# Kernel tuning notes

Measured on AMD Instinct MI355X. Metric: run time of the kernel, lower is better.

Reference implementation:

```python
import jax, jax.numpy as jnp
import numpy as np

N = 2048
T = 4000
MAX_SPIKES = 512
V_RESET = 1.0
ALPHA = 0.01


def setup_inputs() -> dict:
    key = jax.random.key(0)
    k1, k2, k3, k4, k5 = jax.random.split(key, 5)
    ts = jnp.arange(T, dtype=jnp.float32) * (1.0 / T)  # [T] grid over [0, 1)
    v0 = 0.1 * jax.random.normal(k1, (N,), dtype=jnp.float32)
    i0 = 0.1 * jax.random.normal(k2, (N,), dtype=jnp.float32)
    ic = jax.random.uniform(k3, (N,), dtype=jnp.float32, minval=0.5, maxval=1.5)
    # _build_w: uniform weights in [0.5, 1), network mask all-False -> no zeroing
    w = jax.random.uniform(k4, (N, N), dtype=jnp.float32, minval=0.5, maxval=1.0)
    mu = jax.random.uniform(k5, (2,), dtype=jnp.float32, minval=0.5, maxval=1.0)
    return {"ts": ts, "v0": v0, "i0": i0, "ic": ic, "w": w, "mu": mu,
            "seed": 0, "max_spikes": MAX_SPIKES}


def reference(ts, v0, i0, ic, w, mu, seed, max_spikes):
    n = v0.shape[0]
    key = jax.random.key(seed)
    k_init, k_trans = jax.random.split(key)
    # s0 = log(U) - alpha  (negative; spike when s crosses 0)
    s0 = jnp.log(jax.random.uniform(k_init, (n,))) - ALPHA
    y0 = jnp.stack([v0, i0, s0], axis=-1)  # [n, 3]

    dts = ts[1:] - ts[:-1]
    steps = jnp.arange(ts.shape[0] - 1)
    tev0 = jnp.full((max_spikes,), jnp.inf, dtype=ts.dtype)
    yev0 = jnp.full((max_spikes, n, 3), jnp.inf, dtype=y0.dtype)
    et0 = jnp.zeros((max_spikes, n), dtype=bool)

    def drift(y):
        v, i, s = y[:, 0], y[:, 1], y[:, 2]
        dv = mu[0] * (i + ic - v)
        di = -mu[1] * i
        ds = jax.nn.softplus(v)  # intensity_fn
        return jnp.stack([dv, di, ds], axis=-1)

    def step(carry, inp):
        y, nsp, tev, yev, et = carry
        t_next, dt, idx = inp
        y1 = y + dt * drift(y)                 # Euler step
        ev = y1[:, 2] >= 0.0                   # cond_fn: y[n, 2] root crossing
        has = jnp.any(ev)
        eidx = jnp.argmax(ev)
        u = jax.random.uniform(jax.random.fold_in(k_trans, idx), (n,))
        # trans_fn: reset v, add weight row to all i, resample s for spikers
        v_t = y1[:, 0] - jnp.where(ev, V_RESET, 0.0)
        i_t = y1[:, 1] + w[eidx]
        s_t = jnp.where(ev, jnp.log(u) - ALPHA, y1[:, 2])
        y2 = jnp.where(has, jnp.stack([v_t, i_t, s_t], axis=-1), y1)
        rec = has & (nsp < max_spikes)
        widx = jnp.minimum(nsp, max_spikes - 1)
        tev = tev.at[widx].set(jnp.where(rec, t_next, tev[widx]))
        yev = yev.at[widx].set(jnp.where(rec, y1, yev[widx]))
        et = et.at[widx].set(jnp.where(rec, ev, et[widx]))
        nsp = nsp + has.astype(jnp.int32)
        return (y2, nsp, tev, yev, et), y2

    init = (y0, jnp.int32(0), tev0, yev0, et0)
    (_, num_spikes, tevents, yevents, event_types), ys_rest = jax.lax.scan(
        step, init, (ts[1:], dts, steps))
    ys = jnp.concatenate([y0[None], ys_rest], axis=0)  # [T, n, 3]
    return ys, tevents, yevents, event_types, num_spikes
```

## Files before the change

### kernel.cpp

```cpp
#include <hip/hip_runtime.h>
#include <stdint.h>

#define XLA_LOG_TAIL_A 1
#define XLA_USE_FMA    0

#if XLA_USE_FMA
#define MADD(a,b,c) __builtin_fmaf((a),(b),(c))
#else
#define MADD(a,b,c) ((a)*(b)+(c))
#endif

#define N_NEUR 2048
#define HALF_N 1024
#define CKPT   125

#define LDS_BARRIER()                                            \
  do {                                                           \
    __asm__ __volatile__("s_waitcnt lgkmcnt(0)" ::: "memory");   \
    __builtin_amdgcn_s_barrier();                                \
    __asm__ __volatile__("" ::: "memory");                       \
  } while (0)

__device__ __forceinline__ uint32_t rotl32(uint32_t x, int r) {
  return (x << r) | (x >> (32 - r));
}

__device__ __forceinline__ void tf2x32(uint32_t k0, uint32_t k1,
                                       uint32_t& x0, uint32_t& x1) {
  const uint32_t k2 = k0 ^ k1 ^ 0x1BD11BDAu;
  x0 += k0; x1 += k1;
#define TF_R(r) { x0 += x1; x1 = rotl32(x1, r); x1 ^= x0; }
  TF_R(13) TF_R(15) TF_R(26) TF_R(6)
  x0 += k1; x1 += k2 + 1u;
  TF_R(17) TF_R(29) TF_R(16) TF_R(24)
  x0 += k2; x1 += k0 + 2u;
  TF_R(13) TF_R(15) TF_R(26) TF_R(6)
  x0 += k0; x1 += k1 + 3u;
  TF_R(17) TF_R(29) TF_R(16) TF_R(24)
  x0 += k1; x1 += k2 + 4u;
  TF_R(13) TF_R(15) TF_R(26) TF_R(6)
  x0 += k2; x1 += k0 + 5u;
#undef TF_R
}

__device__ __forceinline__ float u01_from_bits(uint32_t bits) {
#pragma clang fp contract(off)
  float f = __uint_as_float((bits >> 9) | 0x3f800000u);
  return f - 1.0f;
}

__device__ __forceinline__ float xla_log(float xin) {
#pragma clang fp contract(off)
  float t0 = fmaxf(xin, __uint_as_float(0x00800000u));
  uint32_t bits = __float_as_uint(t0);
  int em = (int)(bits >> 23) - 127;
  t0 = __uint_as_float((bits & 0x807fffffu) | 0x3f000000u);
  float e = 1.0f + (float)em;
  const bool mlt = t0 < (float)0.707106781186547524;
  float tmp1 = mlt ? t0 : 0.0f;
  t0 = t0 - 1.0f;
  e = e - (mlt ? 1.0f : 0.0f);
  t0 = t0 + tmp1;
  float x2 = t0 * t0;
  float x3 = x2 * t0;
  float y  = MADD(t0, (float)7.0376836292E-2, (float)-1.1514610310E-1);
  float ya = MADD(t0, (float)-1.2420140846E-1, (float)1.4249322787E-1);
  float yb = MADD(t0, (float)2.0000714765E-1, (float)-2.4999993993E-1);
  y  = MADD(y,  t0, (float)1.1676998740E-1);
  ya = MADD(ya, t0, (float)-1.6668057665E-1);
  yb = MADD(yb, t0, (float)3.3333331174E-1);
  y  = MADD(y, x3, ya);
  y  = MADD(y, x3, yb);
  y  = y * x3;
  float ey1 = e * (float)-2.12194440e-4;
  float hx2 = x2 * 0.5f;
  y = y + ey1;
  t0 = t0 - hx2;
  float ey2 = e * (float)0.693359375;
#if XLA_LOG_TAIL_A
  t0 = t0 + y;
  t0 = t0 + ey2;
#else
  t0 = t0 + ey2;
  t0 = t0 + y;
#endif
  if (xin == 0.0f) return -__builtin_inff();
  return t0;
}

__device__ __forceinline__ float xla_exp(float xin) {
#pragma clang fp contract(off)
  float x = fmaxf(xin, (float)-88.3762626647949);
  x = fminf(x, (float)88.3762626647950);
  float fx = floorf(MADD(x, (float)1.44269504088896341, 0.5f));
  float tmp = (float)0.693359375 * fx;
  float z = (float)-2.12194440e-4 * fx;
  x = x - tmp;
  x = x - z;
  z = x * x;
  float y = MADD(x, (float)1.9875691500E-4, (float)1.3981999507E-3);
  y = MADD(y, x, (float)8.3334519073E-3);
  y = MADD(y, x, (float)4.1665795894E-2);
  y = MADD(y, x, (float)1.6666665459E-1);
  y = MADD(y, x, (float)5.0000001201E-1);
  y = MADD(y, z, x);
  y = 1.0f + y;
  int n = (int)fx;
  float p2n = __uint_as_float((uint32_t)(n + 127) << 23);
  return fmaxf(y * p2n, xin);
}

__device__ __forceinline__ float xla_log1p(float x) {
#pragma clang fp contract(off)
  float fl = xla_log(x + 1.0f);
  float fs = ((-0.5f * x) + 1.0f) * x;
  return (fabsf(x) < (float)1e-4) ? fs : fl;
}

__device__ __forceinline__ float softplus_xla(float v) {
#pragma clang fp contract(off)
  if (v >= 16.0f) return v;
  float a = fabsf(v);
  float ex = xla_exp(-a);
  float lp = xla_log1p(ex);
  return fmaxf(v, 0.0f) + lp;
}

__global__ void snn_init(float* __restrict__ out, size_t inf_base,
                         size_t inf_cnt, size_t zero_cnt) {
  size_t i = (size_t)blockIdx.x * blockDim.x + threadIdx.x;
  size_t stride = (size_t)gridDim.x * blockDim.x;
  size_t total = inf_cnt + zero_cnt;
  for (size_t k = i; k < total; k += stride) {
    out[inf_base + k] = (k < inf_cnt) ? __builtin_inff() : 0.0f;
  }
}

__global__ __launch_bounds__(1024)
void snn_pre(const int* __restrict__ seedp, float* __restrict__ sres) {
#pragma clang fp contract(off)
  const int step = blockIdx.x;
  const int t = threadIdx.x;
  uint32_t seed = (uint32_t)seedp[0];
  uint32_t a0 = 0u, a1 = 2u; tf2x32(0u, seed, a0, a1);
  uint32_t b0 = 1u, b1 = 3u; tf2x32(0u, seed, b0, b1);
  uint32_t f0 = 0u, f1 = (uint32_t)step; tf2x32(a1, b1, f0, f1);
  uint32_t d0 = (uint32_t)t, d1 = (uint32_t)(t + HALF_N);
  tf2x32(f0, f1, d0, d1);
  float srA = xla_log(u01_from_bits(d0)) - 0.01f;
  float srB = xla_log(u01_from_bits(d1)) - 0.01f;
  sres[(size_t)step * N_NEUR + t] = srA;
  sres[(size_t)step * N_NEUR + HALF_N + t] = srB;
}

__global__ __launch_bounds__(1024, 1)
void snn_evt(const float* __restrict__ ts, const float* __restrict__ v0,
             const float* __restrict__ i0, const float* __restrict__ ic,
             const float* __restrict__ w, const float* __restrict__ mu,
             const int* __restrict__ seedp, const float* __restrict__ sres,
             uint32_t* __restrict__ spk, float* __restrict__ out, int T, int MS) {
#pragma clang fp contract(off)
  const int tid = threadIdx.x;
  const int nb = tid * 2;
  const int lane = tid & 63;

  float* ys   = out;
  float* tev  = out + (size_t)T * N_NEUR * 3;
  float* yev  = tev + (size_t)MS;
  float* etv  = yev + (size_t)MS * N_NEUR * 3;
  float* nspp = etv + (size_t)MS * N_NEUR;

  uint32_t seed = (uint32_t)seedp[0];
  uint32_t a0 = 0u, a1 = 2u; tf2x32(0u, seed, a0, a1);
  uint32_t b0 = 1u, b1 = 3u; tf2x32(0u, seed, b0, b1);
  const uint32_t ki0 = a0, ki1 = b0;

  float vv0, vv1, ipd0, ipd1, ss0, ss1, icv0, icv1;
  { float2 x = *(const float2*)&v0[nb]; vv0 = x.x; vv1 = x.y; }
  { float2 x = *(const float2*)&i0[nb]; ipd0 = x.x; ipd1 = x.y; }
  { float2 x = *(const float2*)&ic[nb]; icv0 = x.x; icv1 = x.y; }
  {
    uint32_t c0 = (uint32_t)(nb < HALF_N ? nb : nb - HALF_N);
    uint32_t c1 = c0 + HALF_N;
    tf2x32(ki0, ki1, c0, c1);
    ss0 = xla_log(u01_from_bits(nb < HALF_N ? c0 : c1)) - 0.01f;
  }
  {
    int j = nb + 1;
    uint32_t c0 = (uint32_t)(j < HALF_N ? j : j - HALF_N);
    uint32_t c1 = c0 + HALF_N;
    tf2x32(ki0, ki1, c0, c1);
    ss1 = xla_log(u01_from_bits(j < HALF_N ? c0 : c1)) - 0.01f;
  }
  const float m0 = mu[0], m1 = mu[1];

  __shared__ uint32_t slot[4];
  if (tid < 4) slot[tid] = 0xFFFFFFFFu;
  __syncthreads();

  int nsp = 0;
  bool hasPrev = false;
  float wvp0 = 0.0f, wvp1 = 0.0f;
  float tp = ts[0];
  float tn = ts[1];
  const float* srp = sres + nb;
  float sr0, sr1;
  { float2 x = *(const float2*)srp; sr0 = x.x; sr1 = x.y; }
  int next_ck = 0;

  for (int k = 0; k < T - 1; ++k) {
    const float dt = tn - tp;

    float tn_nx = ts[(k + 2 < T) ? (k + 2) : (T - 1)];
    float srn0 = 0.0f, srn1 = 0.0f;
    if (k + 1 < T - 1) {
      float2 x = *(const float2*)(srp + N_NEUR);
      srn0 = x.x; srn1 = x.y;
      srp += N_NEUR;
    }

    float ii0 = hasPrev ? (ipd0 + wvp0) : ipd0;
    float ii1 = hasPrev ? (ipd1 + wvp1) : ipd1;

    if (k == next_ck) {
      float* yr = ys + ((size_t)k * N_NEUR + nb) * 3;
      ((float2*)yr)[0] = make_float2(vv0, ii0);
      ((float2*)yr)[1] = make_float2(ss0, vv1);
      ((float2*)yr)[2] = make_float2(ii1, ss1);
      next_ck += CKPT;
    }

    float sp0 = softplus_xla(vv0);
    float sp1 = softplus_xla(vv1);
    float y1s0 = ss0 + dt * sp0;
    float y1s1 = ss1 + dt * sp1;
    const bool ev0 = (y1s0 >= 0.0f);
    const bool ev1 = (y1s1 >= 0.0f);

    int lidx = ev0 ? 0 : (ev1 ? 1 : 2);
    unsigned long long bm = __ballot(lidx < 2);
    if (lane == 0 && bm) {
      int fl = __builtin_ctzll(bm);
      uint32_t cand = (uint32_t)__builtin_amdgcn_readlane(nb + lidx, fl);
      atomicMin(&slot[k & 3], cand);
    }
    if (tid == 0) slot[(k + 1) & 3] = 0xFFFFFFFFu;

    float dv0 = m0 * ((ii0 + icv0) - vv0);
    float dv1 = m0 * ((ii1 + icv1) - vv1);
    float y1v0 = vv0 + dt * dv0;
    float y1v1 = vv1 + dt * dv1;
    float y1i0 = ii0 + dt * ((-m1) * ii0);
    float y1i1 = ii1 + dt * ((-m1) * ii1);

    LDS_BARRIER();

    uint32_t gmin = (uint32_t)__builtin_amdgcn_readfirstlane((int)slot[k & 3]);
    const bool has = (gmin != 0xFFFFFFFFu);

    float wn0 = 0.0f, wn1 = 0.0f;
    if (has) {
      float2 x = *(const float2*)&w[((size_t)gmin << 11) + nb];
      wn0 = x.x; wn1 = x.y;
    }

    if (tid == 0) {
      spk[k] = ((uint32_t)nsp << 16) | (has ? (gmin & 0xFFFFu) : 0xFFFFu);
      if (has && nsp < MS) tev[nsp] = tn;
    }
    nsp += has ? 1 : 0;

    vv0 = y1v0 - (ev0 ? 1.0f : 0.0f);
    vv1 = y1v1 - (ev1 ? 1.0f : 0.0f);
    ss0 = ev0 ? sr0 : y1s0;
    ss1 = ev1 ? sr1 : y1s1;
    ipd0 = y1i0; ipd1 = y1i1;
    wvp0 = wn0;  wvp1 = wn1;
    hasPrev = has;
    tp = tn; tn = tn_nx;
    sr0 = srn0; sr1 = srn1;
  }

  if (tid == 0) nspp[0] = (float)nsp;
}

__global__ __launch_bounds__(1024, 1)
void snn_rep(const float* __restrict__ ts, const float* __restrict__ ic,
             const float* __restrict__ w, const float* __restrict__ mu,
             const float* __restrict__ sres, const uint32_t* __restrict__ spk,
             float* __restrict__ out, int T, int MS) {
#pragma clang fp contract(off)
  const int seg = blockIdx.x >> 1;
  const int gn = (blockIdx.x & 1) * 1024 + threadIdx.x;
  const int lo = seg * CKPT;
  const int end = min(lo + CKPT, T - 1);

  float* ys  = out;
  float* tev = out + (size_t)T * N_NEUR * 3;
  float* yev = tev + (size_t)MS;
  float* etv = yev + (size_t)MS * N_NEUR * 3;

  const float* y0r = ys + ((size_t)lo * N_NEUR + gn) * 3;
  float vv = y0r[0];
  float ii = y0r[1];
  float ss = y0r[2];
  const float icv = ic[gn];
  const float m0 = mu[0], m1 = mu[1];
  float tp = ts[lo];

  for (int k = lo; k < end; ++k) {
    const float tn = ts[k + 1];
    const float dt = tn - tp;
    tp = tn;
    const uint32_t pk = spk[k];

    float sp  = softplus_xla(vv);
    float y1s = ss + dt * sp;
    const bool ev = (y1s >= 0.0f);
    float dv  = m0 * ((ii + icv) - vv);
    float y1v = vv + dt * dv;
    float y1i = ii + dt * ((-m1) * ii);

    const uint32_t e16 = pk & 0xFFFFu;
    const bool has = (e16 != 0xFFFFu);
    const uint32_t nsp = pk >> 16;

    float wv = 0.0f;
    if (has) wv = w[((size_t)e16 << 11) + gn];

    if (has && nsp < (uint32_t)MS) {
      float* ye = yev + ((size_t)nsp * N_NEUR + gn) * 3;
      ye[0] = y1v; ye[1] = y1i; ye[2] = y1s;
      etv[(size_t)nsp * N_NEUR + gn] = ev ? 1.0f : 0.0f;
    }

    ii = has ? (y1i + wv) : y1i;
    vv = y1v - (ev ? 1.0f : 0.0f);
    if (ev) ss = sres[(size_t)k * N_NEUR + gn]; else ss = y1s;

    float* yr = ys + ((size_t)(k + 1) * N_NEUR + gn) * 3;
    yr[0] = vv; yr[1] = ii; yr[2] = ss;
  }
}

template <bool USE_SRES>
__global__ __launch_bounds__(1024, 1)
void snn_sim(const float* __restrict__ ts, const float* __restrict__ v0,
             const float* __restrict__ i0, const float* __restrict__ ic,
             const float* __restrict__ w, const float* __restrict__ mu,
             const int* __restrict__ seedp, const float* __restrict__ sres,
             float* __restrict__ out, int T, int MS) {
#pragma clang fp contract(off)
  const int tid = threadIdx.x;
  const int nb = tid * 2;
  const int lane = tid & 63;

  float* ys   = out;
  float* tev  = out + (size_t)T * N_NEUR * 3;
  float* yev  = tev + (size_t)MS;
  float* etv  = yev + (size_t)MS * N_NEUR * 3;
  float* nspp = etv + (size_t)MS * N_NEUR;

  uint32_t seed = (uint32_t)seedp[0];
  uint32_t a0 = 0u, a1 = 2u; tf2x32(0u, seed, a0, a1);
  uint32_t b0 = 1u, b1 = 3u; tf2x32(0u, seed, b0, b1);
  const uint32_t ki0 = a0, ki1 = b0;
  const uint32_t kt0 = a1, kt1 = b1;

  float vv0, vv1, ii0, ii1, ss0, ss1, icv0, icv1;
  { float2 x = *(const float2*)&v0[nb]; vv0 = x.x; vv1 = x.y; }
  { float2 x = *(const float2*)&i0[nb]; ii0 = x.x; ii1 = x.y; }
  { float2 x = *(const float2*)&ic[nb]; icv0 = x.x; icv1 = x.y; }
  {
    uint32_t c0 = (uint32_t)(nb < HALF_N ? nb : nb - HALF_N);
    uint32_t c1 = c0 + HALF_N;
    tf2x32(ki0, ki1, c0, c1);
    ss0 = xla_log(u01_from_bits(nb < HALF_N ? c0 : c1)) - 0.01f;
  }
  {
    int j = nb + 1;
    uint32_t c0 = (uint32_t)(j < HALF_N ? j : j - HALF_N);
    uint32_t c1 = c0 + HALF_N;
    tf2x32(ki0, ki1, c0, c1);
    ss1 = xla_log(u01_from_bits(j < HALF_N ? c0 : c1)) - 0.01f;
  }
  const float m0 = mu[0], m1 = mu[1];

  {
    float* yr = ys + (size_t)nb * 3;
    ((float2*)yr)[0] = make_float2(vv0, ii0);
    ((float2*)yr)[1] = make_float2(ss0, vv1);
    ((float2*)yr)[2] = make_float2(ii1, ss1);
  }

  __shared__ uint32_t slot[4];
  if (tid < 4) slot[tid] = 0xFFFFFFFFu;
  __syncthreads();

  int nsp = 0;
  float tp = ts[0];
  const float* srp = USE_SRES ? (sres + nb) : nullptr;
  float* yrow = ys + (size_t)N_NEUR * 3 + (size_t)nb * 3;

  for (int k = 0; k < T - 1; ++k) {
    const float tn = ts[k + 1];
    const float dt = tn - tp;
    tp = tn;

    float sr0 = 0.0f, sr1 = 0.0f;
    if (USE_SRES) {
      float2 x = *(const float2*)srp;
      sr0 = x.x; sr1 = x.y;
      srp += N_NEUR;
    }

    float sp0 = softplus_xla(vv0);
    float sp1 = softplus_xla(vv1);
    float y1s0 = ss0 + dt * sp0;
    float y1s1 = ss1 + dt * sp1;
    const bool ev0 = (y1s0 >= 0.0f);
    const bool ev1 = (y1s1 >= 0.0f);

    int lidx = ev0 ? 0 : (ev1 ? 1 : 2);
    unsigned long long bm = __ballot(lidx < 2);
    if (lane == 0 && bm) {
      int fl = __builtin_ctzll(bm);
      uint32_t cand = (uint32_t)__builtin_amdgcn_readlane(nb + lidx, fl);
      atomicMin(&slot[k & 3], cand);
    }
    if (tid == 0) slot[(k + 1) & 3] = 0xFFFFFFFFu;

    float dv0 = m0 * ((ii0 + icv0) - vv0);
    float dv1 = m0 * ((ii1 + icv1) - vv1);
    float y1v0 = vv0 + dt * dv0;
    float y1v1 = vv1 + dt * dv1;
    float y1i0 = ii0 + dt * ((-m1) * ii0);
    float y1i1 = ii1 + dt * ((-m1) * ii1);

    __syncthreads();

    uint32_t gmin = (uint32_t)__builtin_amdgcn_readfirstlane((int)slot[k & 3]);
    const bool has = (gmin != 0xFFFFFFFFu);

    float wv0 = 0.0f, wv1 = 0.0f;
    if (has) {
      float2 x = *(const float2*)&w[((size_t)gmin << 11) + nb];
      wv0 = x.x; wv1 = x.y;
    }

    if (has && nsp < MS) {
      if (tid == 0) tev[nsp] = tn;
      float* ye = yev + ((size_t)nsp * N_NEUR + nb) * 3;
      ((float2*)ye)[0] = make_float2(y1v0, y1i0);
      ((float2*)ye)[1] = make_float2(y1s0, y1v1);
      ((float2*)ye)[2] = make_float2(y1i1, y1s1);
      *(float2*)(etv + (size_t)nsp * N_NEUR + nb) =
          make_float2(ev0 ? 1.0f : 0.0f, ev1 ? 1.0f : 0.0f);
    }
    nsp += has ? 1 : 0;

    ii0 = has ? (y1i0 + wv0) : y1i0;
    ii1 = has ? (y1i1 + wv1) : y1i1;
    vv0 = y1v0 - (ev0 ? 1.0f : 0.0f);
    vv1 = y1v1 - (ev1 ? 1.0f : 0.0f);
    if (USE_SRES) {
      ss0 = ev0 ? sr0 : y1s0;
      ss1 = ev1 ? sr1 : y1s1;
    } else {
      ss0 = y1s0; ss1 = y1s1;
      if (ev0 | ev1) {
        uint32_t f0 = 0u, f1 = (uint32_t)k;
        tf2x32(kt0, kt1, f0, f1);
        if (ev0) {
          uint32_t c0 = (uint32_t)(nb < HALF_N ? nb : nb - HALF_N);
          uint32_t c1 = c0 + HALF_N;
          tf2x32(f0, f1, c0, c1);
          ss0 = xla_log(u01_from_bits(nb < HALF_N ? c0 : c1)) - 0.01f;
        }
        if (ev1) {
          int j = nb + 1;
          uint32_t c0 = (uint32_t)(j < HALF_N ? j : j - HALF_N);
          uint32_t c1 = c0 + HALF_N;
          tf2x32(f0, f1, c0, c1);
          ss1 = xla_log(u01_from_bits(j < HALF_N ? c0 : c1)) - 0.01f;
        }
      }
    }

    ((float2*)yrow)[0] = make_float2(vv0, ii0);
    ((float2*)yrow)[1] = make_float2(ss0, vv1);
    ((float2*)yrow)[2] = make_float2(ii1, ss1);
    yrow += (size_t)N_NEUR * 3;
  }

  if (tid == 0) nspp[0] = (float)nsp;
}

extern "C" void kernel_launch(void* const* d_in, const int* in_sizes, int n_in,
                              void* d_out, int out_size, void* d_ws, size_t ws_size,
                              hipStream_t stream) {
  const float* ts = (const float*)d_in[0];
  const float* v0 = (const float*)d_in[1];
  const float* i0 = (const float*)d_in[2];
  const float* ic = (const float*)d_in[3];
  const float* w  = (const float*)d_in[4];
  const float* mu = (const float*)d_in[5];
  const int* seed = (const int*)d_in[6];

  const int T = in_sizes[0];
  const int N = in_sizes[1];
  long long rem = (long long)out_size - (long long)T * N * 3 - 1;
  int MS = (int)(rem / (1 + 4 * (long long)N));
  if (MS <= 0) MS = 512;

  size_t inf_base = (size_t)T * N * 3;
  size_t inf_cnt  = (size_t)MS + (size_t)MS * N * 3;
  size_t zero_cnt = (size_t)MS * N;
  snn_init<<<dim3(512), dim3(256), 0, stream>>>((float*)d_out, inf_base, inf_cnt, zero_cnt);

  size_t sres_bytes = (size_t)(T - 1) * (size_t)N * sizeof(float);
  size_t full_bytes = sres_bytes + (size_t)(T - 1) * sizeof(uint32_t);

  if (ws_size >= full_bytes) {
    float* sres = (float*)d_ws;
    uint32_t* spk = (uint32_t*)((char*)d_ws + sres_bytes);
    snn_pre<<<dim3(T - 1), dim3(1024), 0, stream>>>(seed, sres);
    snn_evt<<<dim3(1), dim3(1024), 0, stream>>>(ts, v0, i0, ic, w, mu, seed,
                                                sres, spk, (float*)d_out, T, MS);
    int nseg = (T - 1 + CKPT - 1) / CKPT;
    snn_rep<<<dim3(nseg * 2), dim3(1024), 0, stream>>>(ts, ic, w, mu, sres, spk,
                                                       (float*)d_out, T, MS);
  } else if (ws_size >= sres_bytes) {
    snn_pre<<<dim3(T - 1), dim3(1024), 0, stream>>>(seed, (float*)d_ws);
    snn_sim<true><<<dim3(1), dim3(1024), 0, stream>>>(ts, v0, i0, ic, w, mu, seed,
                                                      (const float*)d_ws,
                                                      (float*)d_out, T, MS);
  } else {
    snn_sim<false><<<dim3(1), dim3(1024), 0, stream>>>(ts, v0, i0, ic, w, mu, seed,
                                                       nullptr, (float*)d_out, T, MS);
  }
}
```

Measured before the change: 3.374 ms.

## Halve event-kernel block to 512 threads with 4 neurons each and per-wave slot reduction

The serial event kernel now runs 512 threads (8 waves) that each own 4 neurons, using float4 loads and stores. The LDS atomicMin slot is replaced by a per-wave slot array that every thread reads and min-reduces after a __syncthreads, double-buffered by step parity. The sres prefetch for the next step is dropped in favour of a direct load in each step. The aim is to cut barrier and atomic cost on the serial critical path, at the price of more per-thread work and a non-prefetched global load inside the loop.

```diff
diff --git a/kernel.cpp b/kernel.cpp
--- a/kernel.cpp
+++ b/kernel.cpp
@@ -13,13 +13,6 @@
 #define N_NEUR 2048
 #define HALF_N 1024
 #define CKPT   125
-
-#define LDS_BARRIER()                                            \
-  do {                                                           \
-    __asm__ __volatile__("s_waitcnt lgkmcnt(0)" ::: "memory");   \
-    __builtin_amdgcn_s_barrier();                                \
-    __asm__ __volatile__("" ::: "memory");                       \
-  } while (0)
 
 __device__ __forceinline__ uint32_t rotl32(uint32_t x, int r) {
   return (x << r) | (x >> (32 - r));
@@ -153,7 +146,7 @@
   sres[(size_t)step * N_NEUR + HALF_N + t] = srB;
 }
 
-__global__ __launch_bounds__(1024, 1)
+__global__ __launch_bounds__(512, 1)
 void snn_evt(const float* __restrict__ ts, const float* __restrict__ v0,
              const float* __restrict__ i0, const float* __restrict__ ic,
              const float* __restrict__ w, const float* __restrict__ mu,
@@ -161,13 +154,13 @@
              uint32_t* __restrict__ spk, float* __restrict__ out, int T, int MS) {
 #pragma clang fp contract(off)
   const int tid = threadIdx.x;
-  const int nb = tid * 2;
+  const int nb = tid * 4;
+  const int wave = tid >> 6;
   const int lane = tid & 63;
 
   float* ys   = out;
   float* tev  = out + (size_t)T * N_NEUR * 3;
-  float* yev  = tev + (size_t)MS;
-  float* etv  = yev + (size_t)MS * N_NEUR * 3;
+  float* etv  = tev + (size_t)MS + (size_t)MS * N_NEUR * 3;
   float* nspp = etv + (size_t)MS * N_NEUR;
 
   uint32_t seed = (uint32_t)seedp[0];
@@ -175,93 +168,112 @@
   uint32_t b0 = 1u, b1 = 3u; tf2x32(0u, seed, b0, b1);
   const uint32_t ki0 = a0, ki1 = b0;
 
-  float vv0, vv1, ipd0, ipd1, ss0, ss1, icv0, icv1;
-  { float2 x = *(const float2*)&v0[nb]; vv0 = x.x; vv1 = x.y; }
-  { float2 x = *(const float2*)&i0[nb]; ipd0 = x.x; ipd1 = x.y; }
-  { float2 x = *(const float2*)&ic[nb]; icv0 = x.x; icv1 = x.y; }
+  float vv[4], ipd[4], ss[4], icv[4], wvp[4];
   {
-    uint32_t c0 = (uint32_t)(nb < HALF_N ? nb : nb - HALF_N);
-    uint32_t c1 = c0 + HALF_N;
-    tf2x32(ki0, ki1, c0, c1);
-    ss0 = xla_log(u01_from_bits(nb < HALF_N ? c0 : c1)) - 0.01f;
+    float4 x = *(const float4*)&v0[nb];
+    vv[0]=x.x; vv[1]=x.y; vv[2]=x.z; vv[3]=x.w;
   }
   {
-    int j = nb + 1;
+    float4 x = *(const float4*)&i0[nb];
+    ipd[0]=x.x; ipd[1]=x.y; ipd[2]=x.z; ipd[3]=x.w;
+  }
+  {
+    float4 x = *(const float4*)&ic[nb];
+    icv[0]=x.x; icv[1]=x.y; icv[2]=x.z; icv[3]=x.w;
+  }
+#pragma unroll
+  for (int q = 0; q < 4; ++q) {
+    int j = nb + q;
     uint32_t c0 = (uint32_t)(j < HALF_N ? j : j - HALF_N);
     uint32_t c1 = c0 + HALF_N;
     tf2x32(ki0, ki1, c0, c1);
-    ss1 = xla_log(u01_from_bits(j < HALF_N ? c0 : c1)) - 0.01f;
+    ss[q] = xla_log(u01_from_bits(j < HALF_N ? c0 : c1)) - 0.01f;
+    wvp[q] = 0.0f;
   }
   const float m0 = mu[0], m1 = mu[1];
 
-  __shared__ uint32_t slot[4];
-  if (tid < 4) slot[tid] = 0xFFFFFFFFu;
+  __shared__ alignas(16) uint32_t slot[2][8];
+  if (tid < 16) ((uint32_t*)slot)[tid] = 0xFFFFFFFFu;
   __syncthreads();
 
   int nsp = 0;
   bool hasPrev = false;
-  float wvp0 = 0.0f, wvp1 = 0.0f;
   float tp = ts[0];
   float tn = ts[1];
-  const float* srp = sres + nb;
-  float sr0, sr1;
-  { float2 x = *(const float2*)srp; sr0 = x.x; sr1 = x.y; }
   int next_ck = 0;
 
   for (int k = 0; k < T - 1; ++k) {
     const float dt = tn - tp;
 
     float tn_nx = ts[(k + 2 < T) ? (k + 2) : (T - 1)];
-    float srn0 = 0.0f, srn1 = 0.0f;
-    if (k + 1 < T - 1) {
-      float2 x = *(const float2*)(srp + N_NEUR);
-      srn0 = x.x; srn1 = x.y;
-      srp += N_NEUR;
-    }
-
-    float ii0 = hasPrev ? (ipd0 + wvp0) : ipd0;
-    float ii1 = hasPrev ? (ipd1 + wvp1) : ipd1;
+    float4 srv = *(const float4*)(sres + (size_t)k * N_NEUR + nb);
+    float sr[4] = {srv.x, srv.y, srv.z, srv.w};
+
+    float ii[4];
+#pragma unroll
+    for (int q = 0; q < 4; ++q) ii[q] = hasPrev ? (ipd[q] + wvp[q]) : ipd[q];
 
     if (k == next_ck) {
       float* yr = ys + ((size_t)k * N_NEUR + nb) * 3;
-      ((float2*)yr)[0] = make_float2(vv0, ii0);
-      ((float2*)yr)[1] = make_float2(ss0, vv1);
-      ((float2*)yr)[2] = make_float2(ii1, ss1);
+      ((float4*)yr)[0] = make_float4(vv[0], ii[0], ss[0], vv[1]);
+      ((float4*)yr)[1] = make_float4(ii[1], ss[1], vv[2], ii[2]);
+      ((float4*)yr)[2] = make_float4(ss[2], vv[3], ii[3], ss[3]);
       next_ck += CKPT;
     }
 
-    float sp0 = softplus_xla(vv0);
-    float sp1 = softplus_xla(vv1);
-    float y1s0 = ss0 + dt * sp0;
-    float y1s1 = ss1 + dt * sp1;
-    const bool ev0 = (y1s0 >= 0.0f);
-    const bool ev1 = (y1s1 >= 0.0f);
-
-    int lidx = ev0 ? 0 : (ev1 ? 1 : 2);
-    unsigned long long bm = __ballot(lidx < 2);
-    if (lane == 0 && bm) {
-      int fl = __builtin_ctzll(bm);
-      uint32_t cand = (uint32_t)__builtin_amdgcn_readlane(nb + lidx, fl);
-      atomicMin(&slot[k & 3], cand);
-    }
-    if (tid == 0) slot[(k + 1) & 3] = 0xFFFFFFFFu;
-
-    float dv0 = m0 * ((ii0 + icv0) - vv0);
-    float dv1 = m0 * ((ii1 + icv1) - vv1);
-    float y1v0 = vv0 + dt * dv0;
-    float y1v1 = vv1 + dt * dv1;
-    float y1i0 = ii0 + dt * ((-m1) * ii0);
-    float y1i1 = ii1 + dt * ((-m1) * ii1);
-
-    LDS_BARRIER();
-
-    uint32_t gmin = (uint32_t)__builtin_amdgcn_readfirstlane((int)slot[k & 3]);
+    float y1s[4];
+    bool ev[4];
+#pragma unroll
+    for (int q = 0; q < 4; ++q) {
+      float sp = softplus_xla(vv[q]);
+      y1s[q] = ss[q] + dt * sp;
+      ev[q] = (y1s[q] >= 0.0f);
+    }
+
+    int lidx = 4;
+    if (ev[3]) lidx = 3;
+    if (ev[2]) lidx = 2;
+    if (ev[1]) lidx = 1;
+    if (ev[0]) lidx = 0;
+    unsigned long long bm = __ballot(lidx < 4);
+    if (lane == 0) {
+      uint32_t cand = 0xFFFFFFFFu;
+      if (bm) {
+        int fl = __builtin_ctzll(bm);
+        cand = (uint32_t)__builtin_amdgcn_readlane(nb + lidx, fl);
+      }
+      slot[k & 1][wave] = cand;
+    }
+
+    float y1v[4], y1i[4];
+#pragma unroll
+    for (int q = 0; q < 4; ++q) {
+      float dv = m0 * ((ii[q] + icv[q]) - vv[q]);
+      y1v[q] = vv[q] + dt * dv;
+      y1i[q] = ii[q] + dt * ((-m1) * ii[q]);
+    }
+
+    __syncthreads();
+
+    uint32_t gmin;
+    {
+      const uint4* rp = (const uint4*)&slot[k & 1][0];
+      uint4 r0 = rp[0], r1 = rp[1];
+      uint32_t a = r0.x < r0.y ? r0.x : r0.y;
+      uint32_t b = r0.z < r0.w ? r0.z : r0.w;
+      uint32_t c = r1.x < r1.y ? r1.x : r1.y;
+      uint32_t d = r1.z < r1.w ? r1.z : r1.w;
+      a = a < b ? a : b;
+      c = c < d ? c : d;
+      gmin = a < c ? a : c;
+    }
+    gmin = (uint32_t)__builtin_amdgcn_readfirstlane((int)gmin);
     const bool has = (gmin != 0xFFFFFFFFu);
 
-    float wn0 = 0.0f, wn1 = 0.0f;
+    float wn[4] = {0.0f, 0.0f, 0.0f, 0.0f};
     if (has) {
-      float2 x = *(const float2*)&w[((size_t)gmin << 11) + nb];
-      wn0 = x.x; wn1 = x.y;
+      float4 x = *(const float4*)&w[((size_t)gmin << 11) + nb];
+      wn[0]=x.x; wn[1]=x.y; wn[2]=x.z; wn[3]=x.w;
     }
 
     if (tid == 0) {
@@ -270,15 +282,15 @@
     }
     nsp += has ? 1 : 0;
 
-    vv0 = y1v0 - (ev0 ? 1.0f : 0.0f);
-    vv1 = y1v1 - (ev1 ? 1.0f : 0.0f);
-    ss0 = ev0 ? sr0 : y1s0;
-    ss1 = ev1 ? sr1 : y1s1;
-    ipd0 = y1i0; ipd1 = y1i1;
-    wvp0 = wn0;  wvp1 = wn1;
+#pragma unroll
+    for (int q = 0; q < 4; ++q) {
+      vv[q] = y1v[q] - (ev[q] ? 1.0f : 0.0f);
+      ss[q] = ev[q] ? sr[q] : y1s[q];
+      ipd[q] = y1i[q];
+      wvp[q] = wn[q];
+    }
     hasPrev = has;
     tp = tn; tn = tn_nx;
-    sr0 = srn0; sr1 = srn1;
   }
 
   if (tid == 0) nspp[0] = (float)nsp;
@@ -525,8 +537,8 @@
     float* sres = (float*)d_ws;
     uint32_t* spk = (uint32_t*)((char*)d_ws + sres_bytes);
     snn_pre<<<dim3(T - 1), dim3(1024), 0, stream>>>(seed, sres);
-    snn_evt<<<dim3(1), dim3(1024), 0, stream>>>(ts, v0, i0, ic, w, mu, seed,
-                                                sres, spk, (float*)d_out, T, MS);
+    snn_evt<<<dim3(1), dim3(512), 0, stream>>>(ts, v0, i0, ic, w, mu, seed,
+                                               sres, spk, (float*)d_out, T, MS);
     int nseg = (T - 1 + CKPT - 1) / CKPT;
     snn_rep<<<dim3(nseg * 2), dim3(1024), 0, stream>>>(ts, ic, w, mu, sres, spk,
                                                        (float*)d_out, T, MS);
```

After: 3.402 ms. About the same (+0.8%).
